# Kernel optimization log

Hardware: AMD Instinct MI355X
Metric: run time of the kernel (lower is better)

The kernel has to match this reference:

```python
import jax, jax.numpy as jnp
import numpy as np

N_NODES = 50000
N_EDGES = 800000
D_NODE = 128
D_EDGE = 16
HID = 64
EPS = 1e-5


def _sage_conv(x, src, dst, Wl, bl, Wr, n_nodes):
    # PyG SAGEConv (mean aggr): out = lin_l(mean_{src->dst} x[src]) + lin_r(x)
    msg = x[src]                                        # [E, F] gather
    s = jax.ops.segment_sum(msg, dst, num_segments=n_nodes)   # [N, F]
    cnt = jax.ops.segment_sum(jnp.ones((src.shape[0],), x.dtype), dst,
                              num_segments=n_nodes)
    agg = s / jnp.maximum(cnt, 1.0)[:, None]
    return agg @ Wl.T + bl + x @ Wr.T


def _batchnorm(h, gamma, beta):
    # training-mode BN over node dim (biased variance, as in torch)
    mu = jnp.mean(h, axis=0)
    var = jnp.mean((h - mu) ** 2, axis=0)
    return gamma * (h - mu) / jnp.sqrt(var + EPS) + beta


def setup_inputs() -> dict:
    key = jax.random.key(0)
    ks = jax.random.split(key, 16)
    def lin(k, out_f, in_f):
        lim = 1.0 / np.sqrt(in_f)
        return jax.random.uniform(k, (out_f, in_f), jnp.float32, -lim, lim)
    x = jax.random.normal(ks[0], (N_NODES, D_NODE), jnp.float32)
    edge_index = jax.random.randint(ks[1], (2, N_EDGES), 0, N_NODES, jnp.int64)
    edge_attr = jax.random.normal(ks[2], (N_EDGES, D_EDGE), jnp.float32)
    return {
        "x": x, "edge_index": edge_index, "edge_attr": edge_attr,
        # SAGEConv 1
        "W1l": lin(ks[3], HID, D_NODE), "b1l": jnp.zeros((HID,), jnp.float32),
        "W1r": lin(ks[4], HID, D_NODE),
        "g1": jnp.ones((HID,), jnp.float32), "be1": jnp.zeros((HID,), jnp.float32),
        # SAGEConv 2
        "W2l": lin(ks[5], HID, HID), "b2l": jnp.zeros((HID,), jnp.float32),
        "W2r": lin(ks[6], HID, HID),
        "g2": jnp.ones((HID,), jnp.float32), "be2": jnp.zeros((HID,), jnp.float32),
        # edge MLP: (2*HID + D_EDGE) -> 128 -> 64 -> 2
        "Wm1": lin(ks[7], 128, 2 * HID + D_EDGE), "bm1": jnp.zeros((128,), jnp.float32),
        "Wm2": lin(ks[8], 64, 128), "bm2": jnp.zeros((64,), jnp.float32),
        "Wm3": lin(ks[9], 2, 64), "bm3": jnp.zeros((2,), jnp.float32),
    }


def reference(x, edge_index, edge_attr,
              W1l, b1l, W1r, g1, be1,
              W2l, b2l, W2r, g2, be2,
              Wm1, bm1, Wm2, bm2, Wm3, bm3):
    src, dst = edge_index[0], edge_index[1]
    n = x.shape[0]
    h = _sage_conv(x, src, dst, W1l, b1l, W1r, n)
    h = jax.nn.relu(_batchnorm(h, g1, be1))          # dropout = identity (eval)
    h = _sage_conv(h, src, dst, W2l, b2l, W2r, n)
    h = jax.nn.relu(_batchnorm(h, g2, be2))
    edge_in = jnp.concatenate([h[src], edge_attr, h[dst]], axis=1)  # [E, 144]
    z = jax.nn.relu(edge_in @ Wm1.T + bm1)
    z = jax.nn.relu(z @ Wm2.T + bm2)
    return z @ Wm3.T + bm3                           # [E, 2] logits
```

## Files before the change

### kernel.cpp

```cpp
#include <hip/hip_runtime.h>
#include <hip/hip_fp16.h>


#define EPS 1e-5f

typedef _Float16 h8 __attribute__((ext_vector_type(8)));
typedef float f32x4 __attribute__((ext_vector_type(4)));

__global__ __launch_bounds__(256) void k_prep_hist(
    const float* __restrict__ W1l, const float* __restrict__ W1r,
    const float* __restrict__ b1l,
    const float* __restrict__ W2l, const float* __restrict__ W2r,
    const float* __restrict__ b2l,
    const float* __restrict__ Wm1, const float* __restrict__ Wm2,
    float* __restrict__ Wt1, float* __restrict__ Wt2,
    float* __restrict__ bias1, float* __restrict__ bias2,
    __half* __restrict__ W2B, __half* __restrict__ W1B,
    const int* __restrict__ dst, int* __restrict__ deg, int E, int prepBlocks) {
  if ((int)blockIdx.x >= prepBlocks) {
    int e = (blockIdx.x - prepBlocks) * 256 + threadIdx.x;
    if (e < E) atomicAdd(&deg[dst[e]], 1);
    return;
  }
  int idx = blockIdx.x * 256 + threadIdx.x;
  if (idx < 16384) {
    int k = idx >> 7, f = idx & 127;
    Wt1[idx] = (f < 64) ? W1l[f * 128 + k] : W1r[(f - 64) * 128 + k];
    return;
  }
  idx -= 16384;
  if (idx < 8192) {
    int k = idx >> 7, f = idx & 127;
    Wt2[idx] = (f < 64) ? W2l[f * 64 + k] : W2r[(f - 64) * 64 + k];
    return;
  }
  idx -= 8192;
  if (idx < 128) { bias1[idx] = (idx < 64) ? 0.f : b1l[idx - 64]; return; }
  idx -= 128;
  if (idx < 128) { bias2[idx] = (idx < 64) ? 0.f : b2l[idx - 64]; return; }
  idx -= 128;
  if (idx < 8192) {
    int j = idx & 7, l = (idx >> 3) & 63, f = idx >> 9;
    int kc = f >> 2, tt = f & 3;
    int col = 16 * tt + (l & 15);
    int k = 32 * kc + (l >> 4) * 8 + j;
    W2B[idx] = __float2half(Wm2[col * 128 + k]);
    return;
  }
  idx -= 8192;
  if (idx < 20480) {
    int j = idx & 7, l = (idx >> 3) & 63, f = idx >> 9;
    int kc = f >> 3, nc = f & 7;
    int k = 32 * kc + (l >> 4) * 8 + j;
    int n = 16 * nc + (l & 15);
    float w;
    if (k < 64)       w = Wm1[n * 144 + k];
    else if (k < 128) w = Wm1[n * 144 + 80 + (k - 64)];
    else if (k < 144) w = Wm1[n * 144 + 64 + (k - 128)];
    else              w = 0.f;
    W1B[idx] = __float2half(w);
    return;
  }
}

__global__ __launch_bounds__(1024) void k_scan(
    const int* __restrict__ deg, int* __restrict__ rowptr,
    int* __restrict__ cursor, int N) {
  __shared__ int wsum[16];
  __shared__ int carry;
  const int lane = threadIdx.x & 63;
  const int w    = threadIdx.x >> 6;
  if (threadIdx.x == 0) carry = 0;
  __syncthreads();
  for (int base = 0; base < N; base += 1024) {
    int i = base + threadIdx.x;
    int v = (i < N) ? deg[i] : 0;
    int incl = v;
#pragma unroll
    for (int off = 1; off < 64; off <<= 1) {
      int t = __shfl_up(incl, off);
      if (lane >= off) incl += t;
    }
    if (lane == 63) wsum[w] = incl;
    __syncthreads();
    if (w == 0) {
      int ws_ = (lane < 16) ? wsum[lane] : 0;
      int wincl = ws_;
#pragma unroll
      for (int off = 1; off < 16; off <<= 1) {
        int t = __shfl_up(wincl, off);
        if (lane >= off) wincl += t;
      }
      if (lane < 16) wsum[lane] = wincl;
    }
    __syncthreads();
    int woff = carry + (w > 0 ? wsum[w - 1] : 0);
    int excl = woff + incl - v;
    if (i < N) { rowptr[i] = excl; cursor[i] = excl; }
    int tot = wsum[15];
    __syncthreads();
    if (threadIdx.x == 0) carry += tot;
    __syncthreads();
  }
  if (threadIdx.x == 0) rowptr[N] = carry;
}

__global__ __launch_bounds__(256) void k_fill(
    const int* __restrict__ src, const int* __restrict__ dst,
    int* __restrict__ cursor, int* __restrict__ csr_src,
    int* __restrict__ csr_dst, int* __restrict__ csr_eid,
    int* __restrict__ pos, int E) {
  int e = blockIdx.x * 256 + threadIdx.x;
  if (e < E) {
    int d = dst[e];
    int p = atomicAdd(&cursor[d], 1);
    csr_src[p] = src[e];
    csr_dst[p] = d;
    csr_eid[p] = e;
    pos[e] = p;
  }
}

__global__ __launch_bounds__(256) void k_scatter_out(
    const float* __restrict__ out2, const int* __restrict__ pos,
    float* __restrict__ out, int E) {
  int e = blockIdx.x * 256 + threadIdx.x;
  if (e < E) {
    int p = pos[e];
    *(float2*)&out[(size_t)e * 2] = *(const float2*)&out2[(size_t)p * 2];
  }
}

template<int K, int MODE>
__global__ __launch_bounds__(256) void k_gemm(
    const float* __restrict__ X, const float* __restrict__ stats,
    const float* __restrict__ Wt, const float* __restrict__ bias,
    __half* __restrict__ outH, float* __restrict__ outF, int N, int Ftot) {
  __shared__ __align__(16) float Xs[32][68];
  __shared__ __align__(16) float Ws_[32][128];
  const int tid = threadIdx.x;
  const int tx  = tid & 15;
  const int ty  = tid >> 4;
  const int n0  = blockIdx.x * 64;
  float acc[4][8];
#pragma unroll
  for (int j = 0; j < 8; ++j) {
    float bv = bias[8 * tx + j];
#pragma unroll
    for (int i = 0; i < 4; ++i) acc[i][j] = bv;
  }
  for (int k0 = 0; k0 < K; k0 += 32) {
    __syncthreads();
#pragma unroll
    for (int l = 0; l < 2; ++l) {
      int idx = tid * 2 + l;
      int kq = idx & 7, n = idx >> 3;
      float4 xv = make_float4(0.f, 0.f, 0.f, 0.f);
      if (n0 + n < N) xv = *(const float4*)&X[(size_t)(n0 + n) * K + k0 + kq * 4];
      if (stats) {
        int kb = k0 + kq * 4;
        xv.x = fmaxf(xv.x * stats[128 + kb + 0] + stats[192 + kb + 0], 0.f);
        xv.y = fmaxf(xv.y * stats[128 + kb + 1] + stats[192 + kb + 1], 0.f);
        xv.z = fmaxf(xv.z * stats[128 + kb + 2] + stats[192 + kb + 2], 0.f);
        xv.w = fmaxf(xv.w * stats[128 + kb + 3] + stats[192 + kb + 3], 0.f);
      }
      Xs[kq * 4 + 0][n] = xv.x;
      Xs[kq * 4 + 1][n] = xv.y;
      Xs[kq * 4 + 2][n] = xv.z;
      Xs[kq * 4 + 3][n] = xv.w;
    }
#pragma unroll
    for (int l = 0; l < 4; ++l) {
      int idx = tid + l * 256;
      int kr = idx >> 5, fc = idx & 31;
      *(float4*)&Ws_[kr][fc * 4] =
          *(const float4*)&Wt[(size_t)(k0 + kr) * Ftot + fc * 4];
    }
    __syncthreads();
#pragma unroll
    for (int kk = 0; kk < 32; ++kk) {
      float4 a  = *(const float4*)&Xs[kk][4 * ty];
      float4 b0 = *(const float4*)&Ws_[kk][8 * tx];
      float4 b1 = *(const float4*)&Ws_[kk][8 * tx + 4];
      float aa[4] = {a.x, a.y, a.z, a.w};
      float bb[8] = {b0.x, b0.y, b0.z, b0.w, b1.x, b1.y, b1.z, b1.w};
#pragma unroll
      for (int i = 0; i < 4; ++i)
#pragma unroll
        for (int j = 0; j < 8; ++j) acc[i][j] += aa[i] * bb[j];
    }
  }
#pragma unroll
  for (int i = 0; i < 4; ++i) {
    int n = n0 + 4 * ty + i;
    if (n >= N) continue;
    if (tx < 8) {
      __half2 hh[4];
#pragma unroll
      for (int c = 0; c < 4; ++c)
        hh[c] = __floats2half2_rn(acc[i][2 * c], acc[i][2 * c + 1]);
      *(uint4*)&outH[(size_t)n * 64 + 8 * tx] = *(uint4*)hh;
    } else {
      float* cp = outF + (size_t)n * 64 + 8 * tx - 64;
      *(float4*)cp = make_float4(acc[i][0], acc[i][1], acc[i][2], acc[i][3]);
      *(float4*)(cp + 4) = make_float4(acc[i][4], acc[i][5], acc[i][6], acc[i][7]);
    }
  }
}

__global__ __launch_bounds__(256) void k_agg(
    const __half* __restrict__ qb, const float* __restrict__ pb,
    const int* __restrict__ rowptr, const int* __restrict__ csr_src,
    float* __restrict__ hpre, float* __restrict__ stats, int N) {
  __shared__ float red[512];
  const int tid  = threadIdx.x;
  const int w    = tid >> 6;
  const int lane = tid & 63;
  const int g    = lane >> 3, c = lane & 7;
  float lsum = 0.f, lsq = 0.f;
  const int wid = blockIdx.x * 4 + w;
  const int nw  = gridDim.x * 4;
  for (int n = wid; n < N; n += nw) {
    const int r0 = rowptr[n], r1 = rowptr[n + 1];
    float s[8] = {0.f, 0.f, 0.f, 0.f, 0.f, 0.f, 0.f, 0.f};
    for (int j = r0 + g; j < r1; j += 8) {
      int a = csr_src[j];
      uint4 rv = *(const uint4*)&qb[(size_t)a * 64 + 8 * c];
      const __half2* hp = (const __half2*)&rv;
#pragma unroll
      for (int q = 0; q < 4; ++q) {
        float2 f2 = __half22float2(hp[q]);
        s[2 * q]     += f2.x;
        s[2 * q + 1] += f2.y;
      }
    }
#pragma unroll
    for (int m = 8; m < 64; m <<= 1)
#pragma unroll
      for (int q = 0; q < 8; ++q) s[q] += __shfl_xor(s[q], m);
    float sv = s[0];
#pragma unroll
    for (int q = 1; q < 8; ++q) sv = (g == q) ? s[q] : sv;
    float cdeg = (float)(r1 - r0);
    cdeg = cdeg > 1.f ? cdeg : 1.f;
    const int f = 8 * c + g;
    float v = sv / cdeg + pb[(size_t)n * 64 + f];
    hpre[(size_t)n * 64 + f] = v;
    lsum += v;
    lsq  += v * v;
  }
  red[tid]       = lsum;
  red[256 + tid] = lsq;
  __syncthreads();
  if (tid < 64) {
    float ts = red[tid] + red[tid + 64] + red[tid + 128] + red[tid + 192];
    float tq = red[256 + tid] + red[256 + tid + 64] + red[256 + tid + 128] + red[256 + tid + 192];
    int f = 8 * (tid & 7) + (tid >> 3);
    atomicAdd(&stats[f], ts);
    atomicAdd(&stats[64 + f], tq);
  }
}

__global__ void k_finalize(float* stats, const float* __restrict__ g,
                           const float* __restrict__ be, int N) {
  int f = threadIdx.x;
  float inv_n = 1.0f / (float)N;
  float mean = stats[f] * inv_n;
  float var  = stats[64 + f] * inv_n - mean * mean;
  float s = g[f] * rsqrtf(var + EPS);
  stats[128 + f] = s;
  stats[192 + f] = be[f] - mean * s;
}

__global__ __launch_bounds__(256) void k_bn(
    const float* __restrict__ H1, const float* __restrict__ stats,
    __half* __restrict__ H2, int N) {
  int idx = blockIdx.x * 256 + threadIdx.x;
  if (idx >= N * 8) return;
  int n = idx >> 3, f8 = (idx & 7) * 8;
  float4 h0 = *(const float4*)&H1[(size_t)n * 64 + f8];
  float4 h1 = *(const float4*)&H1[(size_t)n * 64 + f8 + 4];
  const float* sc = stats + 128 + f8;
  const float* sh = stats + 192 + f8;
  __half2 hh[4];
  hh[0] = __floats2half2_rn(fmaxf(h0.x * sc[0] + sh[0], 0.f),
                            fmaxf(h0.y * sc[1] + sh[1], 0.f));
  hh[1] = __floats2half2_rn(fmaxf(h0.z * sc[2] + sh[2], 0.f),
                            fmaxf(h0.w * sc[3] + sh[3], 0.f));
  hh[2] = __floats2half2_rn(fmaxf(h1.x * sc[4] + sh[4], 0.f),
                            fmaxf(h1.y * sc[5] + sh[5], 0.f));
  hh[3] = __floats2half2_rn(fmaxf(h1.z * sc[6] + sh[6], 0.f),
                            fmaxf(h1.w * sc[7] + sh[7], 0.f));
  *(uint4*)&H2[(size_t)n * 64 + f8] = *(uint4*)hh;
}

__global__ __launch_bounds__(256, 2) void k_edge(
    const __half* __restrict__ H2, const float* __restrict__ attr,
    const int* __restrict__ csrc, const int* __restrict__ cdst,
    const int* __restrict__ ceid,
    const __half* __restrict__ W1Bws, const __half* __restrict__ W2Bws,
    const float* __restrict__ bm1, const float* __restrict__ bm2,
    const float* __restrict__ Wm3, const float* __restrict__ bm3,
    float* __restrict__ out2, int E) {
  __shared__ __align__(16) _Float16 W1B[20480];
  __shared__ __align__(16) _Float16 W2B[8192];
  __shared__ __align__(16) _Float16 Z1f[64 * 136];

  const int tid  = threadIdx.x;
  const int lane = tid & 63;
  const int w    = tid >> 6;
  const int ln15 = lane & 15;
  const int quad = lane >> 4;

  for (int i = tid; i < 2560; i += 256)
    ((uint4*)W1B)[i] = ((const uint4*)W1Bws)[i];
  for (int i = tid; i < 1024; i += 256)
    ((uint4*)W2B)[i] = ((const uint4*)W2Bws)[i];

  float bm1v[8];
#pragma unroll
  for (int nc = 0; nc < 8; ++nc) bm1v[nc] = bm1[16 * nc + ln15];
  float bmv[4], w30[4], w31[4];
#pragma unroll
  for (int t = 0; t < 4; ++t) {
    bmv[t] = bm2[16 * t + ln15];
    w30[t] = Wm3[16 * t + ln15];
    w31[t] = Wm3[64 + 16 * t + ln15];
  }
  const float bm30 = bm3[0], bm31 = bm3[1];
  __syncthreads();

  const int nt = (E + 63) >> 6;
  for (int t = blockIdx.x; t < nt; t += gridDim.x) {
    const int e0 = t << 6;
    int er = e0 + 16 * w + ln15;
    if (er >= E) er = E - 1;
    const int s   = csrc[er];
    const int d   = cdst[er];
    const int eid = ceid[er];

    h8 af[5];
    af[0] = *(const h8*)&H2[(size_t)s * 64 + 8 * quad];
    af[1] = *(const h8*)&H2[(size_t)s * 64 + 32 + 8 * quad];
    af[2] = *(const h8*)&H2[(size_t)d * 64 + 8 * quad];
    af[3] = *(const h8*)&H2[(size_t)d * 64 + 32 + 8 * quad];
    {
      h8 a4 = {0, 0, 0, 0, 0, 0, 0, 0};
      if (quad < 2) {
        float4 f0 = *(const float4*)&attr[(size_t)eid * 16 + 8 * quad];
        float4 f1 = *(const float4*)&attr[(size_t)eid * 16 + 8 * quad + 4];
        a4[0] = (_Float16)f0.x; a4[1] = (_Float16)f0.y;
        a4[2] = (_Float16)f0.z; a4[3] = (_Float16)f0.w;
        a4[4] = (_Float16)f1.x; a4[5] = (_Float16)f1.y;
        a4[6] = (_Float16)f1.z; a4[7] = (_Float16)f1.w;
      }
      af[4] = a4;
    }

    f32x4 acc1[8];
#pragma unroll
    for (int nc = 0; nc < 8; ++nc)
      acc1[nc] = (f32x4){bm1v[nc], bm1v[nc], bm1v[nc], bm1v[nc]};
#pragma unroll
    for (int kc = 0; kc < 5; ++kc)
#pragma unroll
      for (int nc = 0; nc < 8; ++nc) {
        h8 bf = *(const h8*)&W1B[((kc * 8 + nc) << 9) + (lane << 3)];
        acc1[nc] = __builtin_amdgcn_mfma_f32_16x16x32_f16(af[kc], bf, acc1[nc], 0, 0, 0);
      }

    const int ebase = 16 * w + 4 * quad;
#pragma unroll
    for (int nc = 0; nc < 8; ++nc)
#pragma unroll
      for (int r = 0; r < 4; ++r)
        Z1f[(ebase + r) * 136 + 16 * nc + ln15] =
            (_Float16)fmaxf(acc1[nc][r], 0.f);

    f32x4 acc2[4];
#pragma unroll
    for (int tt = 0; tt < 4; ++tt)
      acc2[tt] = (f32x4){bmv[tt], bmv[tt], bmv[tt], bmv[tt]};
#pragma unroll
    for (int kc = 0; kc < 4; ++kc) {
      h8 a = *(const h8*)&Z1f[(16 * w + ln15) * 136 + 32 * kc + 8 * quad];
#pragma unroll
      for (int tt = 0; tt < 4; ++tt) {
        h8 bf = *(const h8*)&W2B[((kc * 4 + tt) * 64 + lane) * 8];
        acc2[tt] = __builtin_amdgcn_mfma_f32_16x16x32_f16(a, bf, acc2[tt], 0, 0, 0);
      }
    }

    float p0[4], p1[4];
#pragma unroll
    for (int r = 0; r < 4; ++r) { p0[r] = 0.f; p1[r] = 0.f; }
#pragma unroll
    for (int tt = 0; tt < 4; ++tt)
#pragma unroll
      for (int r = 0; r < 4; ++r) {
        float z = fmaxf(acc2[tt][r], 0.f);
        p0[r] += z * w30[tt];
        p1[r] += z * w31[tt];
      }
#pragma unroll
    for (int r = 0; r < 4; ++r) {
#pragma unroll
      for (int m = 1; m < 16; m <<= 1) {
        p0[r] += __shfl_xor(p0[r], m);
        p1[r] += __shfl_xor(p1[r], m);
      }
      if (ln15 == 0) {
        int j = e0 + 16 * w + 4 * quad + r;
        if (j < E)
          *(float2*)&out2[(size_t)j * 2] = make_float2(p0[r] + bm30, p1[r] + bm31);
      }
    }
  }
}

extern "C" void kernel_launch(void* const* d_in, const int* in_sizes, int n_in,
                              void* d_out, int out_size, void* d_ws, size_t ws_size,
                              hipStream_t stream) {
  const float* x    = (const float*)d_in[0];
  const int*   ei   = (const int*)d_in[1];
  const float* attr = (const float*)d_in[2];
  const float* W1l  = (const float*)d_in[3];
  const float* b1l  = (const float*)d_in[4];
  const float* W1r  = (const float*)d_in[5];
  const float* g1   = (const float*)d_in[6];
  const float* be1  = (const float*)d_in[7];
  const float* W2l  = (const float*)d_in[8];
  const float* b2l  = (const float*)d_in[9];
  const float* W2r  = (const float*)d_in[10];
  const float* g2   = (const float*)d_in[11];
  const float* be2  = (const float*)d_in[12];
  const float* Wm1  = (const float*)d_in[13];
  const float* bm1  = (const float*)d_in[14];
  const float* Wm2  = (const float*)d_in[15];
  const float* bm2  = (const float*)d_in[16];
  const float* Wm3  = (const float*)d_in[17];
  const float* bm3  = (const float*)d_in[18];
  float* out = (float*)d_out;

  const int N = in_sizes[0] / 128;
  const int E = in_sizes[1] / 2;
  const int* srcI = ei;
  const int* dstI = ei + E;

  float* ws = (float*)d_ws;
  const size_t NF = (size_t)N * 64;
  float*  P32 = ws;
  float*  H1  = ws + NF;
  __half* Q16 = (__half*)(ws + 2 * NF);
  float* small  = ws + 2 * NF + NF / 2;
  float* stats1 = small;
  float* stats2 = stats1 + 256;
  float* Wt1    = stats2 + 256;
  float* Wt2    = Wt1 + 16384;
  float* bias1  = Wt2 + 8192;
  float* bias2  = bias1 + 128;
  __half* W1B   = (__half*)(bias2 + 128);
  __half* W2B   = (__half*)(bias2 + 128 + 10240);
  int* rowptr = (int*)(bias2 + 128 + 10240 + 4096);
  int* cursor = rowptr + (N + 1);
  int* deg    = cursor + N;
  int* csrsrc = deg + N;
  int* csrdst = csrsrc + E;
  int* csreid = csrdst + E;
  int* pos    = csreid + E;

  __half* H2  = Q16;
  float* out2 = H1;

  hipMemsetAsync(deg, 0, (size_t)N * sizeof(int), stream);
  hipMemsetAsync(stats1, 0, 512 * sizeof(float), stream);

  const int eBlocks = (E + 255) / 256;
  const int prepBlocks = (53504 + 255) / 256;
  k_prep_hist<<<prepBlocks + eBlocks, 256, 0, stream>>>(
      W1l, W1r, b1l, W2l, W2r, b2l, Wm1, Wm2,
      Wt1, Wt2, bias1, bias2, W2B, W1B,
      dstI, deg, E, prepBlocks);
  k_scan<<<1, 1024, 0, stream>>>(deg, rowptr, cursor, N);
  k_fill<<<eBlocks, 256, 0, stream>>>(srcI, dstI, cursor, csrsrc, csrdst,
                                      csreid, pos, E);

  const int mTiles = (N + 63) / 64;

  k_gemm<128, 0><<<mTiles, 256, 0, stream>>>(x, nullptr, Wt1, bias1, Q16, P32, N, 128);
  k_agg<<<1024, 256, 0, stream>>>(Q16, P32, rowptr, csrsrc, H1, stats1, N);
  k_finalize<<<1, 64, 0, stream>>>(stats1, g1, be1, N);

  k_gemm<64, 0><<<mTiles, 256, 0, stream>>>(H1, stats1, Wt2, bias2, Q16, P32, N, 128);
  k_agg<<<1024, 256, 0, stream>>>(Q16, P32, rowptr, csrsrc, H1, stats2, N);
  k_finalize<<<1, 64, 0, stream>>>(stats2, g2, be2, N);

  k_bn<<<(N * 8 + 255) / 256, 256, 0, stream>>>(H1, stats2, H2, N);

  k_edge<<<1024, 256, 0, stream>>>(H2, attr, csrsrc, csrdst, csreid,
                                   W1B, W2B, bm1, bm2, Wm3, bm3, out2, E);
  k_scatter_out<<<eBlocks, 256, 0, stream>>>(out2, pos, out, E);
}
```

Baseline: 583.9 us.

## Software-pipeline edge index loads and feature gathers in edge MLP loop

Restructures the persistent edge-MLP loop so the CSR indices for tile t+2G are loaded and the H2/attr gathers for tile t+G are issued before the MFMA work on tile t. This is meant to hide random-gather latency behind compute. It raises register pressure with extra h8 fragments held live, which may lower occupancy. Out-of-range prefetch indices are clamped to E-1, so the extra loads stay in bounds but do redundant work.

```diff
diff --git a/kernel.cpp b/kernel.cpp
--- a/kernel.cpp
+++ b/kernel.cpp
@@ -331,31 +331,46 @@
   __syncthreads();
 
   const int nt = (E + 63) >> 6;
-  for (int t = blockIdx.x; t < nt; t += gridDim.x) {
-    const int e0 = t << 6;
-    int er = e0 + 16 * w + ln15;
-    if (er >= E) er = E - 1;
-    const int s   = csrc[er];
-    const int d   = cdst[er];
-    const int eid = ceid[er];
-
-    h8 af[5];
-    af[0] = *(const h8*)&H2[(size_t)s * 64 + 8 * quad];
-    af[1] = *(const h8*)&H2[(size_t)s * 64 + 32 + 8 * quad];
-    af[2] = *(const h8*)&H2[(size_t)d * 64 + 8 * quad];
-    af[3] = *(const h8*)&H2[(size_t)d * 64 + 32 + 8 * quad];
-    {
-      h8 a4 = {0, 0, 0, 0, 0, 0, 0, 0};
-      if (quad < 2) {
-        float4 f0 = *(const float4*)&attr[(size_t)eid * 16 + 8 * quad];
-        float4 f1 = *(const float4*)&attr[(size_t)eid * 16 + 8 * quad + 4];
-        a4[0] = (_Float16)f0.x; a4[1] = (_Float16)f0.y;
-        a4[2] = (_Float16)f0.z; a4[3] = (_Float16)f0.w;
-        a4[4] = (_Float16)f1.x; a4[5] = (_Float16)f1.y;
-        a4[6] = (_Float16)f1.z; a4[7] = (_Float16)f1.w;
-      }
-      af[4] = a4;
-    }
+  const int G  = gridDim.x;
+  const int rowoff = 16 * w + ln15;
+
+#define LOAD_IDX(t, S, D, EID)                       \
+  {                                                  \
+    int er_ = ((t) << 6) + rowoff;                   \
+    if (er_ >= E) er_ = E - 1;                       \
+    S = csrc[er_]; D = cdst[er_]; EID = ceid[er_];   \
+  }
+
+#define GATHER(S, D, EID, AF)                                          \
+  {                                                                    \
+    AF[0] = *(const h8*)&H2[(size_t)(S) * 64 + 8 * quad];              \
+    AF[1] = *(const h8*)&H2[(size_t)(S) * 64 + 32 + 8 * quad];         \
+    AF[2] = *(const h8*)&H2[(size_t)(D) * 64 + 8 * quad];              \
+    AF[3] = *(const h8*)&H2[(size_t)(D) * 64 + 32 + 8 * quad];         \
+    h8 a4_ = {0, 0, 0, 0, 0, 0, 0, 0};                                 \
+    if (quad < 2) {                                                    \
+      float4 f0_ = *(const float4*)&attr[(size_t)(EID) * 16 + 8 * quad];       \
+      float4 f1_ = *(const float4*)&attr[(size_t)(EID) * 16 + 8 * quad + 4];   \
+      a4_[0] = (_Float16)f0_.x; a4_[1] = (_Float16)f0_.y;              \
+      a4_[2] = (_Float16)f0_.z; a4_[3] = (_Float16)f0_.w;              \
+      a4_[4] = (_Float16)f1_.x; a4_[5] = (_Float16)f1_.y;              \
+      a4_[6] = (_Float16)f1_.z; a4_[7] = (_Float16)f1_.w;              \
+    }                                                                  \
+    AF[4] = a4_;                                                       \
+  }
+
+  int sA, dA, eA, sB, dB, eB;
+  h8 afA[5];
+  const int t0 = blockIdx.x;
+  LOAD_IDX(t0, sA, dA, eA);
+  GATHER(sA, dA, eA, afA);
+  LOAD_IDX(t0 + G, sB, dB, eB);
+
+  for (int t = t0; t < nt; t += G) {
+    int sN, dN, eN;
+    LOAD_IDX(t + 2 * G, sN, dN, eN);
+    h8 afB[5];
+    GATHER(sB, dB, eB, afB);
 
     f32x4 acc1[8];
 #pragma unroll
@@ -366,7 +381,7 @@
 #pragma unroll
       for (int nc = 0; nc < 8; ++nc) {
         h8 bf = *(const h8*)&W1B[((kc * 8 + nc) << 9) + (lane << 3)];
-        acc1[nc] = __builtin_amdgcn_mfma_f32_16x16x32_f16(af[kc], bf, acc1[nc], 0, 0, 0);
+        acc1[nc] = __builtin_amdgcn_mfma_f32_16x16x32_f16(afA[kc], bf, acc1[nc], 0, 0, 0);
       }
 
     const int ebase = 16 * w + 4 * quad;
@@ -410,12 +425,18 @@
         p1[r] += __shfl_xor(p1[r], m);
       }
       if (ln15 == 0) {
-        int j = e0 + 16 * w + 4 * quad + r;
+        int j = (t << 6) + 16 * w + 4 * quad + r;
         if (j < E)
           *(float2*)&out2[(size_t)j * 2] = make_float2(p0[r] + bm30, p1[r] + bm31);
       }
     }
-  }
+
+#pragma unroll
+    for (int i = 0; i < 5; ++i) afA[i] = afB[i];
+    sB = sN; dB = dN; eB = eN;
+  }
+#undef LOAD_IDX
+#undef GATHER
 }
 
 extern "C" void kernel_launch(void* const* d_in, const int* in_sizes, int n_in,
```

After: 610.9 us. 4.6% more time.

## Software-pipeline edge gathers in the edge MLP loop

Applied to the files above, without the earlier changes.

The persistent edge-MLP loop now prefetches the next tile's H2 row fragments and attribute fragment while the current tile's MFMAs run, with edge indices loaded two tiles ahead. This is meant to hide the latency of the dependent random gathers behind compute instead of stalling at the start of every iteration. In exchange it holds more live registers for the prefetched fragments, which may reduce occupancy, and it issues clamped redundant loads past the last tile.

```diff
diff --git a/kernel.cpp b/kernel.cpp
--- a/kernel.cpp
+++ b/kernel.cpp
@@ -331,43 +331,80 @@
   __syncthreads();
 
   const int nt = (E + 63) >> 6;
-  for (int t = blockIdx.x; t < nt; t += gridDim.x) {
-    const int e0 = t << 6;
-    int er = e0 + 16 * w + ln15;
+  const int G  = gridDim.x;
+  const int rowoff = 16 * w + ln15;
+  const int t0 = blockIdx.x;
+
+#define ATTR_FRAG(EID, AF)                                                   \
+  {                                                                          \
+    AF = (h8){0, 0, 0, 0, 0, 0, 0, 0};                                       \
+    if (quad < 2) {                                                          \
+      float4 f0_ = *(const float4*)&attr[(size_t)(EID) * 16 + 8 * quad];     \
+      float4 f1_ = *(const float4*)&attr[(size_t)(EID) * 16 + 8 * quad + 4]; \
+      AF[0] = (_Float16)f0_.x; AF[1] = (_Float16)f0_.y;                      \
+      AF[2] = (_Float16)f0_.z; AF[3] = (_Float16)f0_.w;                      \
+      AF[4] = (_Float16)f1_.x; AF[5] = (_Float16)f1_.y;                      \
+      AF[6] = (_Float16)f1_.z; AF[7] = (_Float16)f1_.w;                      \
+    }                                                                        \
+  }
+
+  int s1, d1, e1i;
+  h8 af0, af1, af2, af3, af4;
+  {
+    int er = (t0 << 6) + rowoff;
     if (er >= E) er = E - 1;
-    const int s   = csrc[er];
-    const int d   = cdst[er];
-    const int eid = ceid[er];
-
-    h8 af[5];
-    af[0] = *(const h8*)&H2[(size_t)s * 64 + 8 * quad];
-    af[1] = *(const h8*)&H2[(size_t)s * 64 + 32 + 8 * quad];
-    af[2] = *(const h8*)&H2[(size_t)d * 64 + 8 * quad];
-    af[3] = *(const h8*)&H2[(size_t)d * 64 + 32 + 8 * quad];
+    int s = csrc[er], d = cdst[er], ei_ = ceid[er];
+    af0 = *(const h8*)&H2[(size_t)s * 64 + 8 * quad];
+    af1 = *(const h8*)&H2[(size_t)s * 64 + 32 + 8 * quad];
+    af2 = *(const h8*)&H2[(size_t)d * 64 + 8 * quad];
+    af3 = *(const h8*)&H2[(size_t)d * 64 + 32 + 8 * quad];
+    ATTR_FRAG(ei_, af4);
+  }
+  {
+    int er = ((t0 + G) << 6) + rowoff;
+    if (er >= E) er = E - 1;
+    s1 = csrc[er]; d1 = cdst[er]; e1i = ceid[er];
+  }
+
+  for (int t = t0; t < nt; t += G) {
+    h8 nf0 = *(const h8*)&H2[(size_t)s1 * 64 + 8 * quad];
+    h8 nf1 = *(const h8*)&H2[(size_t)s1 * 64 + 32 + 8 * quad];
+    h8 nf2 = *(const h8*)&H2[(size_t)d1 * 64 + 8 * quad];
+    h8 nf3 = *(const h8*)&H2[(size_t)d1 * 64 + 32 + 8 * quad];
+
+    f32x4 acc1[8];
+#pragma unroll
+    for (int nc = 0; nc < 8; ++nc)
+      acc1[nc] = (f32x4){bm1v[nc], bm1v[nc], bm1v[nc], bm1v[nc]};
+#pragma unroll
+    for (int nc = 0; nc < 8; ++nc)
+      acc1[nc] = __builtin_amdgcn_mfma_f32_16x16x32_f16(
+          af0, *(const h8*)&W1B[((0 * 8 + nc) << 9) + (lane << 3)], acc1[nc], 0, 0, 0);
+#pragma unroll
+    for (int nc = 0; nc < 8; ++nc)
+      acc1[nc] = __builtin_amdgcn_mfma_f32_16x16x32_f16(
+          af1, *(const h8*)&W1B[((1 * 8 + nc) << 9) + (lane << 3)], acc1[nc], 0, 0, 0);
+#pragma unroll
+    for (int nc = 0; nc < 8; ++nc)
+      acc1[nc] = __builtin_amdgcn_mfma_f32_16x16x32_f16(
+          af2, *(const h8*)&W1B[((2 * 8 + nc) << 9) + (lane << 3)], acc1[nc], 0, 0, 0);
+#pragma unroll
+    for (int nc = 0; nc < 8; ++nc)
+      acc1[nc] = __builtin_amdgcn_mfma_f32_16x16x32_f16(
+          af3, *(const h8*)&W1B[((3 * 8 + nc) << 9) + (lane << 3)], acc1[nc], 0, 0, 0);
+#pragma unroll
+    for (int nc = 0; nc < 8; ++nc)
+      acc1[nc] = __builtin_amdgcn_mfma_f32_16x16x32_f16(
+          af4, *(const h8*)&W1B[((4 * 8 + nc) << 9) + (lane << 3)], acc1[nc], 0, 0, 0);
+
+    h8 nf4;
+    ATTR_FRAG(e1i, nf4);
+    int s2, d2, e2i;
     {
-      h8 a4 = {0, 0, 0, 0, 0, 0, 0, 0};
-      if (quad < 2) {
-        float4 f0 = *(const float4*)&attr[(size_t)eid * 16 + 8 * quad];
-        float4 f1 = *(const float4*)&attr[(size_t)eid * 16 + 8 * quad + 4];
-        a4[0] = (_Float16)f0.x; a4[1] = (_Float16)f0.y;
-        a4[2] = (_Float16)f0.z; a4[3] = (_Float16)f0.w;
-        a4[4] = (_Float16)f1.x; a4[5] = (_Float16)f1.y;
-        a4[6] = (_Float16)f1.z; a4[7] = (_Float16)f1.w;
-      }
-      af[4] = a4;
-    }
-
-    f32x4 acc1[8];
-#pragma unroll
-    for (int nc = 0; nc < 8; ++nc)
-      acc1[nc] = (f32x4){bm1v[nc], bm1v[nc], bm1v[nc], bm1v[nc]};
-#pragma unroll
-    for (int kc = 0; kc < 5; ++kc)
-#pragma unroll
-      for (int nc = 0; nc < 8; ++nc) {
-        h8 bf = *(const h8*)&W1B[((kc * 8 + nc) << 9) + (lane << 3)];
-        acc1[nc] = __builtin_amdgcn_mfma_f32_16x16x32_f16(af[kc], bf, acc1[nc], 0, 0, 0);
-      }
+      int er = ((t + 2 * G) << 6) + rowoff;
+      if (er >= E) er = E - 1;
+      s2 = csrc[er]; d2 = cdst[er]; e2i = ceid[er];
+    }
 
     const int ebase = 16 * w + 4 * quad;
 #pragma unroll
@@ -410,12 +447,16 @@
         p1[r] += __shfl_xor(p1[r], m);
       }
       if (ln15 == 0) {
-        int j = e0 + 16 * w + 4 * quad + r;
+        int j = (t << 6) + 16 * w + 4 * quad + r;
         if (j < E)
           *(float2*)&out2[(size_t)j * 2] = make_float2(p0[r] + bm30, p1[r] + bm31);
       }
     }
-  }
+
+    af0 = nf0; af1 = nf1; af2 = nf2; af3 = nf3; af4 = nf4;
+    s1 = s2; d1 = d2; e1i = e2i;
+  }
+#undef ATTR_FRAG
 }
 
 extern "C" void kernel_launch(void* const* d_in, const int* in_sizes, int n_in,
```

Result: slower. 597.0 us (+2.3%).
